# Kernel optimization log

Measured on AMD Instinct MI355X. Metric: run time of the kernel, lower is better.

The kernel has to match this reference:

```python
import jax, jax.numpy as jnp
import numpy as np


def setup_inputs() -> dict:
    key = jax.random.key(0)
    kx, ky = jax.random.split(key)
    N, M, D = 16384, 16384, 512
    x = jax.random.normal(kx, (N, D), dtype=jnp.float32)
    y = jax.random.normal(ky, (M, D), dtype=jnp.float32)
    return {"x": x, "y": y, "device": 0}


def reference(x, y, device):
    # torch.cdist(x, y, p=2): pairwise Euclidean distances [N, M]
    # matching torch's large-matrix cdist path), clamped for numerical safety.
    x_sq = jnp.sum(x * x, axis=1, keepdims=True)          # [N, 1]
    y_sq = jnp.sum(y * y, axis=1)                          # [M]
    sq_dists = x_sq + y_sq[None, :] - 2.0 * (x @ y.T)      # [N, M]
    dists = jnp.sqrt(jnp.maximum(sq_dists, 0.0))
    # min over centers (dim=1), then argmax over candidates (dim=0)
    min_dists = jnp.min(dists, axis=1)                     # [N]
    max_id = jnp.argmax(min_dists)
    max_val = min_dists[max_id]
    return max_val, max_id
```

## Files before the change

kernel.cpp:

```cpp
#include <hip/hip_runtime.h>
#include <hip/hip_fp8.h>
#include <math.h>

#define N_ROWS 16384
#define M_ROWS 16384
#define DIM    512
#define JS     8
#define KCAND  256
#define DELTA  0.40f

typedef __attribute__((ext_vector_type(8))) int   int8v;
typedef __attribute__((ext_vector_type(4))) int   int4v;
typedef __attribute__((ext_vector_type(4))) float floatx4;

__global__ __launch_bounds__(256) void convert_kernel(const float* __restrict__ x, const float* __restrict__ y,
                                                      unsigned char* __restrict__ xh8, unsigned char* __restrict__ yh8,
                                                      float* __restrict__ x_sq, float* __restrict__ y_sq,
                                                      unsigned int* __restrict__ gmax_bits,
                                                      unsigned int* __restrict__ cnt, int* __restrict__ cand) {
    if (blockIdx.x == 0) {
        if (threadIdx.x < KCAND) cand[threadIdx.x] = 0;
        if (threadIdx.x == 0) { *gmax_bits = 0u; *cnt = 0u; }
    }
    int wave = threadIdx.x >> 6, lane = threadIdx.x & 63;
    int row = blockIdx.x * 4 + wave;
    const float* src; unsigned char* dst8; float* dsq; int r;
    if (row < N_ROWS) { r = row;          src = x; dst8 = xh8; dsq = x_sq; }
    else              { r = row - N_ROWS; src = y; dst8 = yh8; dsq = y_sq; }
    const float4* s4 = (const float4*)(src + (size_t)r * DIM);
    float4 a = s4[lane * 2];
    float4 b = s4[lane * 2 + 1];
    float v[8] = {a.x, a.y, a.z, a.w, b.x, b.y, b.z, b.w};
    union { unsigned char b[8]; uint2 u2; } pk;
    float s = 0.f;
    #pragma unroll
    for (int i = 0; i < 8; ++i) {
        s += v[i] * v[i];
        __hip_fp8_e4m3 q(v[i]);
        pk.b[i] = (unsigned char)q.__x;
    }
    *(uint2*)(dst8 + (size_t)r * DIM + lane * 8) = pk.u2;
    #pragma unroll
    for (int off = 32; off > 0; off >>= 1) s += __shfl_down(s, off, 64);
    if (lane == 0) dsq[r] = s;
}

__device__ __forceinline__ int8v read_frag(const unsigned char* base, int row, int quad) {
    int s = row & 7;
    int c0 = ((quad << 1) | 0) ^ s;
    int c1 = ((quad << 1) | 1) ^ s;
    int4v lo = *(const int4v*)(base + row * 128 + c0 * 16);
    int4v hi = *(const int4v*)(base + row * 128 + c1 * 16);
    int8v r;
    r[0] = lo[0]; r[1] = lo[1]; r[2] = lo[2]; r[3] = lo[3];
    r[4] = hi[0]; r[5] = hi[1]; r[6] = hi[2]; r[7] = hi[3];
    return r;
}

__global__ __launch_bounds__(256) void pass1_kernel(const unsigned char* __restrict__ xh8,
                                                    const unsigned char* __restrict__ yh8,
                                                    const float* __restrict__ y_sq,
                                                    float* __restrict__ part) {
    __shared__ __align__(16) unsigned char As[128 * 128];
    __shared__ __align__(16) unsigned char Bs[128 * 128];
    __shared__ float red[2][128];

    const int t = threadIdx.x;
    const int wid = t >> 6, lane = t & 63;
    const int wm = wid >> 1, wn = wid & 1;
    const int col = lane & 15, quad = lane >> 4;
    const int i0 = blockIdx.x * 128;
    const int jsplit = blockIdx.y;

    const unsigned char* sSrc = (wid < 2) ? xh8 : yh8;
    unsigned char* sDst = (wid < 2) ? As : Bs;
    const int sBase = (wid & 1) * 64;
    const int rr = lane >> 3;
    const int p  = lane & 7;
    const int srcChunkOff = ((p ^ rr) << 4);

    float minv[16];
    #pragma unroll
    for (int i = 0; i < 16; ++i) minv[i] = __builtin_inff();

    for (int jt = 0; jt < (M_ROWS / JS) / 128; ++jt) {
        const int j0 = jsplit * (M_ROWS / JS) + jt * 128;
        const int gBase = (wid < 2) ? i0 : j0;
        floatx4 acc[4][4];
        #pragma unroll
        for (int mt = 0; mt < 4; ++mt)
            #pragma unroll
            for (int nt = 0; nt < 4; ++nt) acc[mt][nt] = (floatx4){0.f, 0.f, 0.f, 0.f};

        for (int kc = 0; kc < DIM; kc += 128) {
            #pragma unroll
            for (int r = 0; r < 8; ++r) {
                const unsigned char* gp = sSrc + (size_t)(gBase + sBase + r * 8 + rr) * DIM + kc + srcChunkOff;
                unsigned char* lp = sDst + (sBase + r * 8) * 128;
                __builtin_amdgcn_global_load_lds((const __attribute__((address_space(1))) void*)gp,
                                                 (__attribute__((address_space(3))) void*)lp, 16, 0, 0);
            }
            __syncthreads();
            int8v afr[4], bfr[4];
            #pragma unroll
            for (int mt = 0; mt < 4; ++mt) afr[mt] = read_frag(As, wm * 64 + mt * 16 + col, quad);
            #pragma unroll
            for (int nt = 0; nt < 4; ++nt) bfr[nt] = read_frag(Bs, wn * 64 + nt * 16 + col, quad);
            #pragma unroll
            for (int mt = 0; mt < 4; ++mt)
                #pragma unroll
                for (int nt = 0; nt < 4; ++nt)
                    acc[mt][nt] = __builtin_amdgcn_mfma_scale_f32_16x16x128_f8f6f4(
                        afr[mt], bfr[nt], acc[mt][nt],
                        0, 0,
                        0, 127,
                        0, 127);
            __syncthreads();
        }
        #pragma unroll
        for (int nt = 0; nt < 4; ++nt) {
            float q = y_sq[j0 + wn * 64 + nt * 16 + col];
            #pragma unroll
            for (int mt = 0; mt < 4; ++mt)
                #pragma unroll
                for (int r = 0; r < 4; ++r)
                    minv[mt * 4 + r] = fminf(minv[mt * 4 + r], q - 2.f * acc[mt][nt][r]);
        }
    }

    #pragma unroll
    for (int i = 0; i < 16; ++i) {
        float v = minv[i];
        v = fminf(v, __shfl_xor(v, 1, 64));
        v = fminf(v, __shfl_xor(v, 2, 64));
        v = fminf(v, __shfl_xor(v, 4, 64));
        v = fminf(v, __shfl_xor(v, 8, 64));
        minv[i] = v;
    }
    if (col == 0) {
        #pragma unroll
        for (int mt = 0; mt < 4; ++mt)
            #pragma unroll
            for (int r = 0; r < 4; ++r)
                red[wn][wm * 64 + mt * 16 + quad * 4 + r] = minv[mt * 4 + r];
    }
    __syncthreads();
    if (t < 128)
        part[(size_t)(i0 + t) * JS + jsplit] = fminf(red[0][t], red[1][t]);
}

__global__ __launch_bounds__(1024) void maxred_kernel(const float* __restrict__ part,
                                                      const float* __restrict__ x_sq,
                                                      float* __restrict__ aval,
                                                      unsigned int* __restrict__ gmax_bits) {
    __shared__ float sm[1024];
    int t = threadIdx.x;
    int row = blockIdx.x * 1024 + t;
    float m = part[(size_t)row * JS];
    #pragma unroll
    for (int c = 1; c < JS; ++c) m = fminf(m, part[(size_t)row * JS + c]);
    float v = sqrtf(fmaxf(x_sq[row] + m, 0.f));
    aval[row] = v;
    sm[t] = v;
    __syncthreads();
    for (int s = 512; s > 0; s >>= 1) {
        if (t < s) sm[t] = fmaxf(sm[t], sm[t + s]);
        __syncthreads();
    }
    if (t == 0) atomicMax(gmax_bits, __float_as_uint(sm[0]));
}

__global__ __launch_bounds__(1024) void select_kernel(const float* __restrict__ aval,
                                                      const unsigned int* __restrict__ gmax_bits,
                                                      unsigned int* __restrict__ cnt,
                                                      int* __restrict__ cand) {
    int row = blockIdx.x * 1024 + threadIdx.x;
    float gmax = __uint_as_float(*gmax_bits);
    if (aval[row] >= gmax - DELTA) {
        unsigned s = atomicAdd(cnt, 1u);
        if (s < KCAND) cand[s] = row;
    }
}

#define TIr 64
#define LDA 68
#define LDB 132
__global__ __launch_bounds__(256) void rescore_kernel(const float* __restrict__ x, const float* __restrict__ y,
                                                      const float* __restrict__ y_sq,
                                                      const int* __restrict__ cand,
                                                      const unsigned int* __restrict__ cnt,
                                                      float* __restrict__ part2) {
    __shared__ __align__(16) float As[32 * LDA];
    __shared__ __align__(16) float Bs[32 * LDB];
    __shared__ float red[TIr][17];

    int t = threadIdx.x;
    int tx = t & 15, ty = t >> 4;
    int i0 = blockIdx.x * TIr;
    int j0 = blockIdx.y * 128;

    if ((unsigned)i0 >= *cnt) return;

    float acc[4][8];
    #pragma unroll
    for (int c = 0; c < 4; ++c)
        #pragma unroll
        for (int d = 0; d < 8; ++d) acc[c][d] = 0.f;

    int srow = t >> 3;
    int skq = (t & 7) * 4;
    int grow0 = cand[i0 + srow];
    int grow1 = cand[i0 + 32 + srow];

    for (int kc = 0; kc < DIM; kc += 32) {
        {
            float4 v = *(const float4*)(x + (size_t)grow0 * DIM + kc + skq);
            As[(skq + 0) * LDA + srow] = v.x;
            As[(skq + 1) * LDA + srow] = v.y;
            As[(skq + 2) * LDA + srow] = v.z;
            As[(skq + 3) * LDA + srow] = v.w;
            v = *(const float4*)(x + (size_t)grow1 * DIM + kc + skq);
            As[(skq + 0) * LDA + 32 + srow] = v.x;
            As[(skq + 1) * LDA + 32 + srow] = v.y;
            As[(skq + 2) * LDA + 32 + srow] = v.z;
            As[(skq + 3) * LDA + 32 + srow] = v.w;
        }
        #pragma unroll
        for (int it = 0; it < 4; ++it) {
            int row = it * 32 + srow;
            float4 v = *(const float4*)(y + (size_t)(j0 + row) * DIM + kc + skq);
            Bs[(skq + 0) * LDB + row] = v.x;
            Bs[(skq + 1) * LDB + row] = v.y;
            Bs[(skq + 2) * LDB + row] = v.z;
            Bs[(skq + 3) * LDB + row] = v.w;
        }
        __syncthreads();
        #pragma unroll 8
        for (int k = 0; k < 32; ++k) {
            float4 a  = *(const float4*)&As[k * LDA + ty * 4];
            float4 b0 = *(const float4*)&Bs[k * LDB + tx * 8];
            float4 b1 = *(const float4*)&Bs[k * LDB + tx * 8 + 4];
            float av[4] = {a.x, a.y, a.z, a.w};
            float bv[8] = {b0.x, b0.y, b0.z, b0.w, b1.x, b1.y, b1.z, b1.w};
            #pragma unroll
            for (int c = 0; c < 4; ++c)
                #pragma unroll
                for (int d = 0; d < 8; ++d)
                    acc[c][d] = fmaf(av[c], bv[d], acc[c][d]);
        }
        __syncthreads();
    }

    float4 q0 = *(const float4*)(y_sq + j0 + tx * 8);
    float4 q1 = *(const float4*)(y_sq + j0 + tx * 8 + 4);
    float qv[8] = {q0.x, q0.y, q0.z, q0.w, q1.x, q1.y, q1.z, q1.w};
    float mv[4] = {__builtin_inff(), __builtin_inff(), __builtin_inff(), __builtin_inff()};
    #pragma unroll
    for (int c = 0; c < 4; ++c)
        #pragma unroll
        for (int d = 0; d < 8; ++d)
            mv[c] = fminf(mv[c], qv[d] - 2.f * acc[c][d]);
    #pragma unroll
    for (int c = 0; c < 4; ++c) red[ty * 4 + c][tx] = mv[c];
    __syncthreads();
    if (t < TIr) {
        float m = red[t][0];
        #pragma unroll
        for (int xx = 1; xx < 16; ++xx) m = fminf(m, red[t][xx]);
        part2[(size_t)(i0 + t) * 128 + blockIdx.y] = m;
    }
}

__global__ __launch_bounds__(256) void final2_kernel(const float* __restrict__ part2,
                                                     const float* __restrict__ x_sq,
                                                     const int* __restrict__ cand,
                                                     const unsigned int* __restrict__ cnt,
                                                     float* __restrict__ out) {
    __shared__ float sv[256];
    __shared__ int si[256];
    int t = threadIdx.x;
    const float4* p4 = (const float4*)(part2 + (size_t)t * 128);
    float m = __builtin_inff();
    for (int c = 0; c < 32; ++c) {
        float4 v = p4[c];
        m = fminf(m, fminf(fminf(v.x, v.y), fminf(v.z, v.w)));
    }
    unsigned n = *cnt;
    if (n > KCAND) n = KCAND;
    int row = cand[t];
    float v = (t < (int)n) ? sqrtf(fmaxf(x_sq[row] + m, 0.f)) : -__builtin_inff();
    sv[t] = v; si[t] = row;
    __syncthreads();
    for (int s = 128; s > 0; s >>= 1) {
        if (t < s) {
            float v2 = sv[t + s]; int i2 = si[t + s];
            if (v2 > sv[t] || (v2 == sv[t] && i2 < si[t])) { sv[t] = v2; si[t] = i2; }
        }
        __syncthreads();
    }
    if (t == 0) { out[0] = sv[0]; out[1] = (float)si[0]; }
}

extern "C" void kernel_launch(void* const* d_in, const int* in_sizes, int n_in,
                              void* d_out, int out_size, void* d_ws, size_t ws_size,
                              hipStream_t stream) {
    const float* x = (const float*)d_in[0];
    const float* y = (const float*)d_in[1];
    float* out = (float*)d_out;

    char* w = (char*)d_ws;
    unsigned char* xh8 = (unsigned char*)w;
    unsigned char* yh8 = (unsigned char*)(w + (size_t)8388608);
    float* x_sq = (float*)(w + (size_t)16777216);
    float* y_sq = x_sq + N_ROWS;
    float* part = y_sq + M_ROWS;
    float* aval = part + (size_t)N_ROWS * JS;
    float* part2 = aval + N_ROWS;
    int* cand = (int*)(part2 + KCAND * 128);
    unsigned int* gmax_bits = (unsigned int*)(cand + KCAND);
    unsigned int* cnt = gmax_bits + 1;

    convert_kernel<<<(N_ROWS + M_ROWS) / 4, 256, 0, stream>>>(x, y, xh8, yh8, x_sq, y_sq, gmax_bits, cnt, cand);
    dim3 g1(N_ROWS / 128, JS);
    pass1_kernel<<<g1, 256, 0, stream>>>(xh8, yh8, y_sq, part);
    maxred_kernel<<<N_ROWS / 1024, 1024, 0, stream>>>(part, x_sq, aval, gmax_bits);
    select_kernel<<<N_ROWS / 1024, 1024, 0, stream>>>(aval, gmax_bits, cnt, cand);
    dim3 g2(KCAND / TIr, M_ROWS / 128);
    rescore_kernel<<<g2, 256, 0, stream>>>(x, y, y_sq, cand, cnt, part2);
    final2_kernel<<<1, 256, 0, stream>>>(part2, x_sq, cand, cnt, out);
}
```

Measured before the change: 310.2 us.

## Widen pass1 N-tile to 256, shrink rescore tiles and reduction blocks

The FP8 MFMA pass now handles 256 y-rows per iteration instead of 128. Each wave computes a 64x128 sub-tile with 32 accumulators, so A fragments are reused across twice as many MFMAs and the number of LDS loads and syncs per output drops. The rescore kernel is retiled to 16 candidate rows per block, so blocks whose rows fall past the candidate count exit early and wasted FP32 work on sparse candidates is cut. The max-reduction kernel reads part with float4 loads, and it and the select kernel now use 256-thread blocks. The risks are higher register pressure (128 accumulator VGPRs) and more LDS per block, which may lower occupancy in pass1.

```diff
diff --git a/kernel.cpp b/kernel.cpp
--- a/kernel.cpp
+++ b/kernel.cpp
@@ -62,7 +62,7 @@
                                                     const float* __restrict__ y_sq,
                                                     float* __restrict__ part) {
     __shared__ __align__(16) unsigned char As[128 * 128];
-    __shared__ __align__(16) unsigned char Bs[128 * 128];
+    __shared__ __align__(16) unsigned char Bs[256 * 128];
     __shared__ float red[2][128];
 
     const int t = threadIdx.x;
@@ -72,9 +72,6 @@
     const int i0 = blockIdx.x * 128;
     const int jsplit = blockIdx.y;
 
-    const unsigned char* sSrc = (wid < 2) ? xh8 : yh8;
-    unsigned char* sDst = (wid < 2) ? As : Bs;
-    const int sBase = (wid & 1) * 64;
     const int rr = lane >> 3;
     const int p  = lane & 7;
     const int srcChunkOff = ((p ^ rr) << 4);
@@ -83,43 +80,54 @@
     #pragma unroll
     for (int i = 0; i < 16; ++i) minv[i] = __builtin_inff();
 
-    for (int jt = 0; jt < (M_ROWS / JS) / 128; ++jt) {
-        const int j0 = jsplit * (M_ROWS / JS) + jt * 128;
-        const int gBase = (wid < 2) ? i0 : j0;
-        floatx4 acc[4][4];
+    for (int jt = 0; jt < (M_ROWS / JS) / 256; ++jt) {
+        const int j0 = jsplit * (M_ROWS / JS) + jt * 256;
+        floatx4 acc[4][8];
         #pragma unroll
         for (int mt = 0; mt < 4; ++mt)
             #pragma unroll
-            for (int nt = 0; nt < 4; ++nt) acc[mt][nt] = (floatx4){0.f, 0.f, 0.f, 0.f};
+            for (int nt = 0; nt < 8; ++nt) acc[mt][nt] = (floatx4){0.f, 0.f, 0.f, 0.f};
 
         for (int kc = 0; kc < DIM; kc += 128) {
             #pragma unroll
+            for (int r = 0; r < 4; ++r) {
+                const unsigned char* gp = xh8 + (size_t)(i0 + wid * 32 + r * 8 + rr) * DIM + kc + srcChunkOff;
+                unsigned char* lp = As + (wid * 32 + r * 8) * 128;
+                __builtin_amdgcn_global_load_lds((const __attribute__((address_space(1))) void*)gp,
+                                                 (__attribute__((address_space(3))) void*)lp, 16, 0, 0);
+            }
+            #pragma unroll
             for (int r = 0; r < 8; ++r) {
-                const unsigned char* gp = sSrc + (size_t)(gBase + sBase + r * 8 + rr) * DIM + kc + srcChunkOff;
-                unsigned char* lp = sDst + (sBase + r * 8) * 128;
+                const unsigned char* gp = yh8 + (size_t)(j0 + wid * 64 + r * 8 + rr) * DIM + kc + srcChunkOff;
+                unsigned char* lp = Bs + (wid * 64 + r * 8) * 128;
                 __builtin_amdgcn_global_load_lds((const __attribute__((address_space(1))) void*)gp,
                                                  (__attribute__((address_space(3))) void*)lp, 16, 0, 0);
             }
             __syncthreads();
-            int8v afr[4], bfr[4];
+            int8v afr[4];
             #pragma unroll
             for (int mt = 0; mt < 4; ++mt) afr[mt] = read_frag(As, wm * 64 + mt * 16 + col, quad);
             #pragma unroll
-            for (int nt = 0; nt < 4; ++nt) bfr[nt] = read_frag(Bs, wn * 64 + nt * 16 + col, quad);
-            #pragma unroll
-            for (int mt = 0; mt < 4; ++mt)
+            for (int h = 0; h < 2; ++h) {
+                int8v bfr[4];
                 #pragma unroll
-                for (int nt = 0; nt < 4; ++nt)
-                    acc[mt][nt] = __builtin_amdgcn_mfma_scale_f32_16x16x128_f8f6f4(
-                        afr[mt], bfr[nt], acc[mt][nt],
-                        0, 0,
-                        0, 127,
-                        0, 127);
+                for (int n = 0; n < 4; ++n)
+                    bfr[n] = read_frag(Bs, wn * 128 + (h * 4 + n) * 16 + col, quad);
+                #pragma unroll
+                for (int mt = 0; mt < 4; ++mt)
+                    #pragma unroll
+                    for (int n = 0; n < 4; ++n)
+                        acc[mt][h * 4 + n] = __builtin_amdgcn_mfma_scale_f32_16x16x128_f8f6f4(
+                            afr[mt], bfr[n], acc[mt][h * 4 + n],
+                            0, 0,
+                            0, 127,
+                            0, 127);
+            }
             __syncthreads();
         }
         #pragma unroll
-        for (int nt = 0; nt < 4; ++nt) {
-            float q = y_sq[j0 + wn * 64 + nt * 16 + col];
+        for (int nt = 0; nt < 8; ++nt) {
+            float q = y_sq[j0 + wn * 128 + nt * 16 + col];
             #pragma unroll
             for (int mt = 0; mt < 4; ++mt)
                 #pragma unroll
@@ -149,32 +157,33 @@
         part[(size_t)(i0 + t) * JS + jsplit] = fminf(red[0][t], red[1][t]);
 }
 
-__global__ __launch_bounds__(1024) void maxred_kernel(const float* __restrict__ part,
-                                                      const float* __restrict__ x_sq,
-                                                      float* __restrict__ aval,
-                                                      unsigned int* __restrict__ gmax_bits) {
-    __shared__ float sm[1024];
+__global__ __launch_bounds__(256) void maxred_kernel(const float* __restrict__ part,
+                                                     const float* __restrict__ x_sq,
+                                                     float* __restrict__ aval,
+                                                     unsigned int* __restrict__ gmax_bits) {
+    __shared__ float sm[256];
     int t = threadIdx.x;
-    int row = blockIdx.x * 1024 + t;
-    float m = part[(size_t)row * JS];
-    #pragma unroll
-    for (int c = 1; c < JS; ++c) m = fminf(m, part[(size_t)row * JS + c]);
+    int row = blockIdx.x * 256 + t;
+    float4 p0 = *(const float4*)(part + (size_t)row * JS);
+    float4 p1 = *(const float4*)(part + (size_t)row * JS + 4);
+    float m = fminf(fminf(fminf(p0.x, p0.y), fminf(p0.z, p0.w)),
+                    fminf(fminf(p1.x, p1.y), fminf(p1.z, p1.w)));
     float v = sqrtf(fmaxf(x_sq[row] + m, 0.f));
     aval[row] = v;
     sm[t] = v;
     __syncthreads();
-    for (int s = 512; s > 0; s >>= 1) {
+    for (int s = 128; s > 0; s >>= 1) {
         if (t < s) sm[t] = fmaxf(sm[t], sm[t + s]);
         __syncthreads();
     }
     if (t == 0) atomicMax(gmax_bits, __float_as_uint(sm[0]));
 }
 
-__global__ __launch_bounds__(1024) void select_kernel(const float* __restrict__ aval,
-                                                      const unsigned int* __restrict__ gmax_bits,
-                                                      unsigned int* __restrict__ cnt,
-                                                      int* __restrict__ cand) {
-    int row = blockIdx.x * 1024 + threadIdx.x;
+__global__ __launch_bounds__(256) void select_kernel(const float* __restrict__ aval,
+                                                     const unsigned int* __restrict__ gmax_bits,
+                                                     unsigned int* __restrict__ cnt,
+                                                     int* __restrict__ cand) {
+    int row = blockIdx.x * 256 + threadIdx.x;
     float gmax = __uint_as_float(*gmax_bits);
     if (aval[row] >= gmax - DELTA) {
         unsigned s = atomicAdd(cnt, 1u);
@@ -182,48 +191,40 @@
     }
 }
 
-#define TIr 64
-#define LDA 68
 #define LDB 132
 __global__ __launch_bounds__(256) void rescore_kernel(const float* __restrict__ x, const float* __restrict__ y,
                                                       const float* __restrict__ y_sq,
                                                       const int* __restrict__ cand,
                                                       const unsigned int* __restrict__ cnt,
                                                       float* __restrict__ part2) {
-    __shared__ __align__(16) float As[32 * LDA];
+    __shared__ float As[32 * 16];
     __shared__ __align__(16) float Bs[32 * LDB];
-    __shared__ float red[TIr][17];
+    __shared__ float red[16][33];
 
     int t = threadIdx.x;
-    int tx = t & 15, ty = t >> 4;
-    int i0 = blockIdx.x * TIr;
+    int tx = t & 31, ty = t >> 5;
+    int i0 = blockIdx.x * 16;
     int j0 = blockIdx.y * 128;
 
     if ((unsigned)i0 >= *cnt) return;
 
-    float acc[4][8];
-    #pragma unroll
-    for (int c = 0; c < 4; ++c)
-        #pragma unroll
-        for (int d = 0; d < 8; ++d) acc[c][d] = 0.f;
+    float acc[2][4];
+    #pragma unroll
+    for (int c = 0; c < 2; ++c)
+        #pragma unroll
+        for (int d = 0; d < 4; ++d) acc[c][d] = 0.f;
 
     int srow = t >> 3;
-    int skq = (t & 7) * 4;
-    int grow0 = cand[i0 + srow];
-    int grow1 = cand[i0 + 32 + srow];
+    int skq  = (t & 7) * 4;
+    int arow = cand[i0 + (srow & 15)];
 
     for (int kc = 0; kc < DIM; kc += 32) {
-        {
-            float4 v = *(const float4*)(x + (size_t)grow0 * DIM + kc + skq);
-            As[(skq + 0) * LDA + srow] = v.x;
-            As[(skq + 1) * LDA + srow] = v.y;
-            As[(skq + 2) * LDA + srow] = v.z;
-            As[(skq + 3) * LDA + srow] = v.w;
-            v = *(const float4*)(x + (size_t)grow1 * DIM + kc + skq);
-            As[(skq + 0) * LDA + 32 + srow] = v.x;
-            As[(skq + 1) * LDA + 32 + srow] = v.y;
-            As[(skq + 2) * LDA + 32 + srow] = v.z;
-            As[(skq + 3) * LDA + 32 + srow] = v.w;
+        if (t < 128) {
+            float4 v = *(const float4*)(x + (size_t)arow * DIM + kc + skq);
+            As[(skq + 0) * 16 + srow] = v.x;
+            As[(skq + 1) * 16 + srow] = v.y;
+            As[(skq + 2) * 16 + srow] = v.z;
+            As[(skq + 3) * 16 + srow] = v.w;
         }
         #pragma unroll
         for (int it = 0; it < 4; ++it) {
@@ -237,36 +238,34 @@
         __syncthreads();
         #pragma unroll 8
         for (int k = 0; k < 32; ++k) {
-            float4 a  = *(const float4*)&As[k * LDA + ty * 4];
-            float4 b0 = *(const float4*)&Bs[k * LDB + tx * 8];
-            float4 b1 = *(const float4*)&Bs[k * LDB + tx * 8 + 4];
-            float av[4] = {a.x, a.y, a.z, a.w};
-            float bv[8] = {b0.x, b0.y, b0.z, b0.w, b1.x, b1.y, b1.z, b1.w};
-            #pragma unroll
-            for (int c = 0; c < 4; ++c)
-                #pragma unroll
-                for (int d = 0; d < 8; ++d)
-                    acc[c][d] = fmaf(av[c], bv[d], acc[c][d]);
+            float a0 = As[k * 16 + ty * 2];
+            float a1 = As[k * 16 + ty * 2 + 1];
+            float4 b = *(const float4*)&Bs[k * LDB + tx * 4];
+            float bv[4] = {b.x, b.y, b.z, b.w};
+            #pragma unroll
+            for (int d = 0; d < 4; ++d) {
+                acc[0][d] = fmaf(a0, bv[d], acc[0][d]);
+                acc[1][d] = fmaf(a1, bv[d], acc[1][d]);
+            }
         }
         __syncthreads();
     }
 
-    float4 q0 = *(const float4*)(y_sq + j0 + tx * 8);
-    float4 q1 = *(const float4*)(y_sq + j0 + tx * 8 + 4);
-    float qv[8] = {q0.x, q0.y, q0.z, q0.w, q1.x, q1.y, q1.z, q1.w};
-    float mv[4] = {__builtin_inff(), __builtin_inff(), __builtin_inff(), __builtin_inff()};
-    #pragma unroll
-    for (int c = 0; c < 4; ++c)
-        #pragma unroll
-        for (int d = 0; d < 8; ++d)
+    float4 q = *(const float4*)(y_sq + j0 + tx * 4);
+    float qv[4] = {q.x, q.y, q.z, q.w};
+    float mv[2] = {__builtin_inff(), __builtin_inff()};
+    #pragma unroll
+    for (int c = 0; c < 2; ++c)
+        #pragma unroll
+        for (int d = 0; d < 4; ++d)
             mv[c] = fminf(mv[c], qv[d] - 2.f * acc[c][d]);
     #pragma unroll
-    for (int c = 0; c < 4; ++c) red[ty * 4 + c][tx] = mv[c];
+    for (int c = 0; c < 2; ++c) red[ty * 2 + c][tx] = mv[c];
     __syncthreads();
-    if (t < TIr) {
+    if (t < 16) {
         float m = red[t][0];
         #pragma unroll
-        for (int xx = 1; xx < 16; ++xx) m = fminf(m, red[t][xx]);
+        for (int xx = 1; xx < 32; ++xx) m = fminf(m, red[t][xx]);
         part2[(size_t)(i0 + t) * 128 + blockIdx.y] = m;
     }
 }
@@ -316,16 +315,16 @@
     float* part = y_sq + M_ROWS;
     float* aval = part + (size_t)N_ROWS * JS;
     float* part2 = aval + N_ROWS;
-    int* cand = (int*)(part2 + KCAND * 128);
+    int* cand = (int*)(part2 + (size_t)KCAND * 128);
     unsigned int* gmax_bits = (unsigned int*)(cand + KCAND);
     unsigned int* cnt = gmax_bits + 1;
 
     convert_kernel<<<(N_ROWS + M_ROWS) / 4, 256, 0, stream>>>(x, y, xh8, yh8, x_sq, y_sq, gmax_bits, cnt, cand);
     dim3 g1(N_ROWS / 128, JS);
     pass1_kernel<<<g1, 256, 0, stream>>>(xh8, yh8, y_sq, part);
-    maxred_kernel<<<N_ROWS / 1024, 1024, 0, stream>>>(part, x_sq, aval, gmax_bits);
-    select_kernel<<<N_ROWS / 1024, 1024, 0, stream>>>(aval, gmax_bits, cnt, cand);
-    dim3 g2(KCAND / TIr, M_ROWS / 128);
+    maxred_kernel<<<N_ROWS / 256, 256, 0, stream>>>(part, x_sq, aval, gmax_bits);
+    select_kernel<<<N_ROWS / 256, 256, 0, stream>>>(aval, gmax_bits, cnt, cand);
+    dim3 g2(KCAND / 16, M_ROWS / 128);
     rescore_kernel<<<g2, 256, 0, stream>>>(x, y, y_sq, cand, cnt, part2);
     final2_kernel<<<1, 256, 0, stream>>>(part2, x_sq, cand, cnt, out);
 }
```

New measurement: 388.6 us. +25.2%, slower.
